# Kernel optimization log

Measured on AMD Instinct MI355X. Metric: run time of the kernel, lower is better.

## Reference

```python
import jax, jax.numpy as jnp
import numpy as np

T, B, IN = 256, 64, 512
HIDDEN = [512, 512, 512]
DILATIONS = [1, 2, 4]


def _lstm_scan(x, W_ih, W_hh, b_ih, b_hh):
    """Run an LSTMCell over leading time axis of x: [Td, N, D] -> [Td, N, H]."""
    H = W_hh.shape[1]
    N = x.shape[1]
    h0 = jnp.zeros((N, H), x.dtype)
    c0 = jnp.zeros((N, H), x.dtype)

    def step(carry, xt):
        h, c = carry
        gates = xt @ W_ih.T + b_ih + h @ W_hh.T + b_hh  # [N, 4H], torch order i,f,g,o
        i, f, g, o = jnp.split(gates, 4, axis=-1)
        c = jax.nn.sigmoid(f) * c + jax.nn.sigmoid(i) * jnp.tanh(g)
        h = jax.nn.sigmoid(o) * jnp.tanh(c)
        return (h, c), h

    _, hs = jax.lax.scan(step, (h0, c0), x)
    return hs


def _drnn_layer(x, rate, W_ih, W_hh, b_ih, b_hh):
    """Dilated RNN layer. x: [T, B, D] with T % rate == 0.
    Torch code concats `rate` consecutive timesteps along batch -> one dilated step;
    reshape [T,B,D] -> [T//rate, rate*B, D] reproduces exactly that layout, and the
    chunk/unroll at the end is the inverse reshape."""
    Tn, Bn, D = x.shape
    Td = Tn // rate
    xd = x.reshape(Td, rate * Bn, D)
    hs = _lstm_scan(xd, W_ih, W_hh, b_ih, b_hh)  # [Td, rate*B, H]
    return hs.reshape(Tn, Bn, W_hh.shape[1])


def setup_inputs() -> dict:
    key = jax.random.key(0)
    ks = jax.random.split(key, 1 + 4 * len(HIDDEN))
    inp = {"x": jax.random.normal(ks[0], (T, B, IN), dtype=jnp.float32)}
    in_dim = IN
    ki = 1
    for li, H in enumerate(HIDDEN):
        bound = 1.0 / np.sqrt(H)
        inp[f"W_ih{li}"] = jax.random.uniform(ks[ki + 0], (4 * H, in_dim), jnp.float32, -bound, bound)
        inp[f"W_hh{li}"] = jax.random.uniform(ks[ki + 1], (4 * H, H), jnp.float32, -bound, bound)
        inp[f"b_ih{li}"] = jax.random.uniform(ks[ki + 2], (4 * H,), jnp.float32, -bound, bound)
        inp[f"b_hh{li}"] = jax.random.uniform(ks[ki + 3], (4 * H,), jnp.float32, -bound, bound)
        ki += 4
        in_dim = H
    return inp


def reference(x,
              W_ih0, W_hh0, b_ih0, b_hh0,
              W_ih1, W_hh1, b_ih1, b_hh1,
              W_ih2, W_hh2, b_ih2, b_hh2):
    params = [(W_ih0, W_hh0, b_ih0, b_hh0),
              (W_ih1, W_hh1, b_ih1, b_hh1),
              (W_ih2, W_hh2, b_ih2, b_hh2)]
    h = x
    for (Wih, Whh, bih, bhh), rate in zip(params, DILATIONS):
        h = _drnn_layer(h, rate, Wih, Whh, bih, bhh)
    return h  # [T, B, HIDDEN[-1]]
```

## Files before the change

### kernel.cpp

```cpp
#include <hip/hip_runtime.h>

typedef __attribute__((ext_vector_type(8))) short bf16x8;
typedef __attribute__((ext_vector_type(4))) float f32x4;

__device__ __forceinline__ unsigned short f2bf(float x) {
    unsigned u = __float_as_uint(x);
    u += 0x7FFFu + ((u >> 16) & 1u);
    return (unsigned short)(u >> 16);
}
__device__ __forceinline__ float sigm(float x) { return 1.0f / (1.0f + __expf(-x)); }
__device__ __forceinline__ float ftanh(float x) {
    float e = __expf(2.f * x);
    return 1.f - 2.f / (e + 1.f);
}

__device__ __forceinline__ void gld16(const unsigned short* g, unsigned short* l) {
    __builtin_amdgcn_global_load_lds((const __attribute__((address_space(1))) void*)g,
                                     (__attribute__((address_space(3))) void*)l, 16, 0, 0);
}

__device__ __forceinline__ void st_plain32(unsigned* p, unsigned v) {
    asm volatile("global_store_dword %0, %1, off" :: "v"(p), "v"(v) : "memory");
}
__device__ __forceinline__ void st_wt32(unsigned* p, unsigned v) {
    asm volatile("global_store_dword %0, %1, off sc0 sc1" :: "v"(p), "v"(v) : "memory");
}
__device__ __forceinline__ void aaddMALL(unsigned* p) {
    unsigned one = 1;
    asm volatile("global_atomic_add %0, %1, off sc1" :: "v"(p), "v"(one) : "memory");
}
__device__ __forceinline__ unsigned ld_mall(const unsigned* p) {
    unsigned v;
    asm volatile("global_load_dword %0, %1, off sc0 sc1\n\ts_waitcnt vmcnt(0)"
                 : "=v"(v) : "v"(p) : "memory");
    return v;
}
__device__ __forceinline__ void st_wt16(unsigned short* p, unsigned v) {
    asm volatile("global_store_short %0, %1, off sc0 sc1" :: "v"(p), "v"(v) : "memory");
}

__device__ __forceinline__ float dppx1(float x) {
    return __int_as_float(__builtin_amdgcn_mov_dpp(__float_as_int(x), 0xB1, 0xF, 0xF, true));
}
__device__ __forceinline__ float dppx2(float x) {
    return __int_as_float(__builtin_amdgcn_mov_dpp(__float_as_int(x), 0x4E, 0xF, 0xF, true));
}

__global__ __launch_bounds__(256) void k_conv_x(const float* __restrict__ x,
                                                unsigned short* __restrict__ Xp) {
    int i = blockIdx.x * 256 + threadIdx.x;
    int rb = i >> 10, kc = (i >> 6) & 15, ln = i & 63;
    int row = (rb << 4) + (ln & 15);
    int k   = (kc << 5) + ((ln >> 4) << 3);
    const float* s = x + (size_t)row * 512 + k;
    float4 v0 = *(const float4*)s, v1 = *(const float4*)(s + 4);
    unsigned short o[8] = {f2bf(v0.x), f2bf(v0.y), f2bf(v0.z), f2bf(v0.w),
                           f2bf(v1.x), f2bf(v1.y), f2bf(v1.z), f2bf(v1.w)};
    *(bf16x8*)(Xp + (size_t)i * 8) = *(bf16x8*)o;
}

__global__ __launch_bounds__(256) void k_conv_w(const float* __restrict__ Wih,
                                                const float* __restrict__ Whh,
                                                unsigned short* __restrict__ Wp) {
    int i = blockIdx.x * 256 + threadIdx.x;
    int wrb = i >> 11, kc = (i >> 6) & 31, ln = i & 63;
    int j = (wrb << 4) + (ln & 15);
    int k = (kc << 5) + ((ln >> 4) << 3);
    int srow = (j & 3) * 512 + (j >> 2);
    const float* s = (k < 512) ? (Wih + (size_t)srow * 512 + k)
                               : (Whh + (size_t)srow * 512 + (k - 512));
    float4 v0 = *(const float4*)s, v1 = *(const float4*)(s + 4);
    unsigned short o[8] = {f2bf(v0.x), f2bf(v0.y), f2bf(v0.z), f2bf(v0.w),
                           f2bf(v1.x), f2bf(v1.y), f2bf(v1.z), f2bf(v1.w)};
    *(bf16x8*)(Wp + (size_t)i * 8) = *(bf16x8*)o;
}

struct DP {
    const unsigned short* Xp;
    unsigned short *Hp0, *Hp1, *Hp2;
    unsigned short *Xq1, *Xq2;
    const unsigned short *Wp0, *Wp1, *Wp2;
    const float *bi0, *bh0, *bi1, *bh1, *bi2, *bh2;
    float* Out;
    unsigned int* flags;
};

__device__ __forceinline__ void quadT(f32x4 a, int sq, float& G0, float& G1, float& G2, float& G3) {
    float a0 = a[0], a1 = a[1], a2 = a[2], a3 = a[3];
    float p1 = (sq & 1) ? a0 : a1; float g1_ = dppx1(p1);
    float p2 = (sq & 1) ? a2 : a3; float g2_ = dppx1(p2);
    float m0 = (sq & 1) ? g1_ : a0, m1 = (sq & 1) ? a1 : g1_;
    float m2 = (sq & 1) ? g2_ : a2, m3 = (sq & 1) ? a3 : g2_;
    float q1 = (sq & 2) ? m0 : m2; float h1_ = dppx2(q1);
    float q2 = (sq & 2) ? m1 : m3; float h2_ = dppx2(q2);
    G0 = (sq & 2) ? h1_ : m0; G1 = (sq & 2) ? h2_ : m1;
    G2 = (sq & 2) ? m2 : h1_; G3 = (sq & 2) ? m3 : h2_;
}

#define PIN8(A,B,C,D,E,F,G,H) \
    asm volatile("" : "+v"(A),"+v"(B),"+v"(C),"+v"(D),"+v"(E),"+v"(F),"+v"(G),"+v"(H))
#define SBAR()  __builtin_amdgcn_sched_barrier(0)
#define MEMBAR() asm volatile("" ::: "memory")
#define RAWBAR() do { MEMBAR(); SBAR(); __builtin_amdgcn_s_barrier(); SBAR(); MEMBAR(); } while (0)

__global__ __launch_bounds__(256, 1) void k_drnn(DP p) {
    const int tid = threadIdx.x, lane = tid & 63, wv = tid >> 6;
    const int l15 = lane & 15, lhi = lane >> 4, sq = l15 & 3;

    const int b = blockIdx.x;
    const int cid = b & 7, w = b >> 3;
    int l, c, T, P, N;
    if (cid < 2)      { l = 0; c = cid;     T = 256; P = 1; N = 64;  }
    else if (cid < 4) { l = 1; c = cid - 2; T = 128; P = 2; N = 128; }
    else              { l = 2; c = cid - 4; T = 64;  P = 2; N = 256; }

    const unsigned short* Xs = (l == 0) ? p.Xp  : (l == 1 ? p.Xq1 : p.Xq2);
    unsigned short*       Hd = (l == 0) ? p.Hp0 : (l == 1 ? p.Hp1 : p.Hp2);
    unsigned short*       Xw = (l == 0) ? p.Xq1 : (l == 1 ? p.Xq2 : nullptr);
    const unsigned short* Ws = (l == 0) ? p.Wp0 : (l == 1 ? p.Wp1 : p.Wp2);
    const float* bi = (l == 0) ? p.bi0 : (l == 1 ? p.bi1 : p.bi2);
    const float* bh = (l == 0) ? p.bh0 : (l == 1 ? p.bh1 : p.bh2);
    const int R0 = c * (P * 32);
    const int alias = (p.Xq1 == p.Hp0);

    __shared__ unsigned short At[65536];
    __shared__ unsigned pollbuf[32];

    const unsigned short* wbase = Ws + ((size_t)(((w << 2) + wv) * 32) << 9) + lane * 8;
#define DECLW(n) bf16x8 w##n = *(const bf16x8*)(wbase + (n << 9));
    DECLW(0) DECLW(1) DECLW(2) DECLW(3) DECLW(4) DECLW(5) DECLW(6) DECLW(7)
    DECLW(8) DECLW(9) DECLW(10) DECLW(11) DECLW(12) DECLW(13) DECLW(14) DECLW(15)
    DECLW(16) DECLW(17) DECLW(18) DECLW(19) DECLW(20) DECLW(21) DECLW(22) DECLW(23)
    DECLW(24) DECLW(25) DECLW(26) DECLW(27) DECLW(28) DECLW(29) DECLW(30) DECLW(31)

    const int hcol = (w << 4) + (wv << 2) + (l15 >> 2);
    const float bs0 = bi[hcol]        + bh[hcol];
    const float bs1 = bi[512 + hcol]  + bh[512 + hcol];
    const float bs2 = bi[1024 + hcol] + bh[1024 + hcol];
    const float bs3 = bi[1536 + hcol] + bh[1536 + hcol];

    const int kch = hcol >> 5;
    const int lane16 = (((hcol & 31) >> 3) << 4) + ((lhi << 2) + sq);
    const int st_lt = lane16 * 8 + (hcol & 7);

    float cst0 = 0.f, cst1 = 0.f, cst2 = 0.f, cst3 = 0.f;
    unsigned int* iflagV = p.flags;
    unsigned int* mflagV = p.flags + 256;
    unsigned int* cflagS = p.flags + 512;
    int fastok = 1;

#define KPX(na, nb, E0, E1, O0, O1, A0, A1) { \
    bf16x8 xa = *(const bf16x8*)((A0) + ((na) << 9)); \
    bf16x8 xb = *(const bf16x8*)((A1) + ((na) << 9)); \
    bf16x8 ya = *(const bf16x8*)((A0) + ((nb) << 9)); \
    bf16x8 yb = *(const bf16x8*)((A1) + ((nb) << 9)); \
    E0 = __builtin_amdgcn_mfma_f32_16x16x32_bf16(xa, w##na, E0, 0, 0, 0); \
    E1 = __builtin_amdgcn_mfma_f32_16x16x32_bf16(xb, w##na, E1, 0, 0, 0); \
    O0 = __builtin_amdgcn_mfma_f32_16x16x32_bf16(ya, w##nb, O0, 0, 0, 0); \
    O1 = __builtin_amdgcn_mfma_f32_16x16x32_bf16(yb, w##nb, O1, 0, 0, 0); }

#define XH(E0, E1, O0, O1, A0, A1) \
    KPX(0,1,E0,E1,O0,O1,A0,A1) KPX(2,3,E0,E1,O0,O1,A0,A1) \
    KPX(4,5,E0,E1,O0,O1,A0,A1) KPX(6,7,E0,E1,O0,O1,A0,A1) \
    KPX(8,9,E0,E1,O0,O1,A0,A1) KPX(10,11,E0,E1,O0,O1,A0,A1) \
    KPX(12,13,E0,E1,O0,O1,A0,A1) KPX(14,15,E0,E1,O0,O1,A0,A1)
#define HH(E0, E1, O0, O1, A0, A1) \
    KPX(16,17,E0,E1,O0,O1,A0,A1) KPX(18,19,E0,E1,O0,O1,A0,A1) \
    KPX(20,21,E0,E1,O0,O1,A0,A1) KPX(22,23,E0,E1,O0,O1,A0,A1) \
    KPX(24,25,E0,E1,O0,O1,A0,A1) KPX(26,27,E0,E1,O0,O1,A0,A1) \
    KPX(28,29,E0,E1,O0,O1,A0,A1) KPX(30,31,E0,E1,O0,O1,A0,A1)

#define PWC(RV, CSTV, HV) { \
    float G0, G1, G2, G3; quadT(RV, sq, G0, G1, G2, G3); \
    float cn = sigm(G1 + bs1) * CSTV + sigm(G0 + bs0) * ftanh(G2 + bs2); \
    HV = sigm(G3 + bs3) * ftanh(cn); CSTV = cn; }

#define STAGE_X(TT) { \
    const int RxN = ((TT) * N + R0) >> 4; \
    for (int i = 0; i < P * 8; ++i) { \
        int q = wv * (P * 8) + i, rb = q >> 4, kc = q & 15; \
        gld16(Xs + ((size_t)((RxN + rb) * 16 + kc) << 9) + lane * 8, \
              &At[(rb * 32 + kc) << 9]); } }
#define STAGE_H(TT) { \
    const int RhN = ((TT) * N + R0) >> 4; \
    for (int i = 0; i < P * 8; ++i) { \
        int q = wv * (P * 8) + i, rb = q >> 4, kc = q & 15; \
        gld16(Hd + ((size_t)((RhN + rb) * 16 + kc) << 9) + lane * 8, \
              &At[(rb * 32 + 16 + kc) << 9]); } }

#define CPOLL(TT) { \
    if (l == 1 && wv == 1 && lane < 2) { \
        const unsigned* cp = cflagS + lane * 32; \
        const unsigned need = 32u * (unsigned)(2 * (TT) + c + 1); \
        int n = 0; \
        while (!__all(ld_mall(cp) >= need)) { if (++n > (1 << 22)) break; } \
    } \
    if (l == 2 && wv == 1 && lane == 0) { \
        const unsigned* cp = cflagS + (2 + (c & 1)) * 32; \
        const unsigned need = 32u * (unsigned)(2 * (TT) + (c >> 1) + 1); \
        int n = 0; \
        while (ld_mall(cp) < need) { if (++n > (1 << 22)) break; } \
    } }

    f32x4 e0 = {0,0,0,0}, e1 = {0,0,0,0}, o0 = {0,0,0,0}, o1 = {0,0,0,0};
    f32x4 e2 = {0,0,0,0}, e3 = {0,0,0,0}, o2 = {0,0,0,0}, o3 = {0,0,0,0};
    const unsigned short* A00 = At + lane * 8;
    const unsigned short* A01 = A00 + (32 << 9);
    const unsigned short* A10 = A00 + (64 << 9);
    const unsigned short* A11 = A00 + (96 << 9);

    if (l > 0) CPOLL(0);
    RAWBAR();
    STAGE_X(0);
    asm volatile("s_waitcnt vmcnt(0)" ::: "memory");
    RAWBAR();
    { XH(e0, e1, o0, o1, A00, A01) }
    if (P == 2) { XH(e2, e3, o2, o3, A10, A11) }

    for (int t = 0; t < T; ++t) {
        PIN8(w0,w1,w2,w3,w4,w5,w6,w7);
        PIN8(w8,w9,w10,w11,w12,w13,w14,w15);
        PIN8(w16,w17,w18,w19,w20,w21,w22,w23);
        PIN8(w24,w25,w26,w27,w28,w29,w30,w31);

        const int RxB = (t * N + R0) >> 4;

        if (t > 0) {
            if (wv == 0) {
                const unsigned need = (unsigned)t;
                const unsigned* mp = mflagV + cid * 32 + (lane & 31);
                if (t == T - 1 || !fastok) {
                    int n = 0;
                    while (!__all(ld_mall(mp) >= need)) { if (++n > (1 << 22)) break; }
                } else {
                    const unsigned short* gip = (const unsigned short*)(iflagV + cid * 32);
                    volatile unsigned* pb = pollbuf;
                    int n = 0;
                    for (;;) {
                        if (lane < 8) gld16(gip + lane * 8, (unsigned short*)pollbuf);
                        asm volatile("s_waitcnt vmcnt(0)" ::: "memory");
                        SBAR();
                        unsigned v = pb[lane & 31];
                        if (__all((v - need) <= 1u)) break;
                        if (++n > 1024) {
                            fastok = 0;
                            int m = 0;
                            while (!__all(ld_mall(mp) >= need)) { if (++m > (1 << 22)) break; }
                            break;
                        }
                    }
                }
            }
            RAWBAR();
            STAGE_H(t - 1);
            asm volatile("s_waitcnt vmcnt(0)" ::: "memory");
            RAWBAR();
            { HH(e0, e1, o0, o1, A00, A01) }
            if (P == 2) { HH(e2, e3, o2, o3, A10, A11) }
        }

        float hv0, hv1, hv2 = 0.f, hv3 = 0.f;
        { f32x4 r0 = e0 + o0, r1 = e1 + o1;
          PWC(r0, cst0, hv0) PWC(r1, cst1, hv1) }
        if (P == 2) {
          f32x4 r2 = e2 + o2, r3 = e3 + o3;
          PWC(r2, cst2, hv2) PWC(r3, cst3, hv3) }

        const unsigned short hb0 = f2bf(hv0), hb1 = f2bf(hv1);
        const unsigned short hb2 = f2bf(hv2), hb3 = f2bf(hv3);
        const size_t i0 = ((size_t)((RxB + 0) * 16 + kch) << 9) + st_lt;
        const size_t i1 = ((size_t)((RxB + 1) * 16 + kch) << 9) + st_lt;
        const size_t i2 = ((size_t)((RxB + 2) * 16 + kch) << 9) + st_lt;
        const size_t i3 = ((size_t)((RxB + 3) * 16 + kch) << 9) + st_lt;
        if (!alias || l == 2) {
            Hd[i0] = hb0; Hd[i1] = hb1;
            if (P == 2) { Hd[i2] = hb2; Hd[i3] = hb3; }
        }
        if (l == 2) {
            p.Out[((size_t)(((RxB + 0) << 4) + (lhi << 2) + sq)) * 512 + hcol] = hv0;
            p.Out[((size_t)(((RxB + 1) << 4) + (lhi << 2) + sq)) * 512 + hcol] = hv1;
            p.Out[((size_t)(((RxB + 2) << 4) + (lhi << 2) + sq)) * 512 + hcol] = hv2;
            p.Out[((size_t)(((RxB + 3) << 4) + (lhi << 2) + sq)) * 512 + hcol] = hv3;
        }
        MEMBAR(); SBAR();
        if (l == 0) { st_wt16(Xw + i0, hb0); st_wt16(Xw + i1, hb1); }
        else if (l == 1) { st_wt16(Xw + i0, hb0); st_wt16(Xw + i1, hb1);
                           st_wt16(Xw + i2, hb2); st_wt16(Xw + i3, hb3); }
        SBAR();
        if (alias && l < 2)  asm volatile("s_waitcnt vmcnt(0)" ::: "memory");
        else if (l == 0)     asm volatile("s_waitcnt vmcnt(2)" ::: "memory");
        else                 asm volatile("s_waitcnt vmcnt(4)" ::: "memory");
        RAWBAR();

        if (t + 1 < T) {
            if (l == 0) {
                STAGE_X(t + 1);
                MEMBAR(); SBAR();
                if (tid == 192) {
                    st_plain32(iflagV + cid * 32 + w, (unsigned)(t + 1));
                    st_wt32(mflagV + cid * 32 + w, (unsigned)(t + 1));
                }
                if (tid == 128 && t > 0) aaddMALL(cflagS + cid * 32);
                SBAR();
                if (wv == 3)                asm volatile("s_waitcnt vmcnt(2)" ::: "memory");
                else if (wv == 2 && t > 0)  asm volatile("s_waitcnt vmcnt(1)" ::: "memory");
                else                        asm volatile("s_waitcnt vmcnt(0)" ::: "memory");
            } else {
                if (tid == 192) {
                    st_plain32(iflagV + cid * 32 + w, (unsigned)(t + 1));
                    st_wt32(mflagV + cid * 32 + w, (unsigned)(t + 1));
                }
                if (tid == 128 && l == 1 && t > 0) aaddMALL(cflagS + cid * 32);
                CPOLL(t + 1);
                RAWBAR();
                STAGE_X(t + 1);
                asm volatile("s_waitcnt vmcnt(0)" ::: "memory");
            }
            RAWBAR();
            e0 = (f32x4){0,0,0,0}; e1 = (f32x4){0,0,0,0};
            o0 = (f32x4){0,0,0,0}; o1 = (f32x4){0,0,0,0};
            { XH(e0, e1, o0, o1, A00, A01) }
            if (P == 2) {
                e2 = (f32x4){0,0,0,0}; e3 = (f32x4){0,0,0,0};
                o2 = (f32x4){0,0,0,0}; o3 = (f32x4){0,0,0,0};
                XH(e2, e3, o2, o3, A10, A11)
            }
        }
    }

    asm volatile("s_waitcnt vmcnt(0)" ::: "memory");
    __builtin_amdgcn_s_barrier();
    if (tid == 192) {
        st_plain32(iflagV + cid * 32 + w, (unsigned)T);
        st_wt32(mflagV + cid * 32 + w, (unsigned)T);
    }
    if (tid == 128 && l < 2) {
        aaddMALL(cflagS + cid * 32);
        aaddMALL(cflagS + cid * 32);
    }
}

extern "C" void kernel_launch(void* const* d_in, const int* in_sizes, int n_in,
                              void* d_out, int out_size, void* d_ws, size_t ws_size,
                              hipStream_t stream)
{
    const float* x = (const float*)d_in[0];
    const float* Wih[3] = {(const float*)d_in[1], (const float*)d_in[5], (const float*)d_in[9]};
    const float* Whh[3] = {(const float*)d_in[2], (const float*)d_in[6], (const float*)d_in[10]};
    const float* bih[3] = {(const float*)d_in[3], (const float*)d_in[7], (const float*)d_in[11]};
    const float* bhh[3] = {(const float*)d_in[4], (const float*)d_in[8], (const float*)d_in[12]};

    char* wp = (char*)d_ws;
    const size_t SZ_A = (size_t)16384 * 512;
    unsigned int* flags = (unsigned int*)wp; wp += 4096;
    unsigned short* Xp  = (unsigned short*)wp; wp += SZ_A * 2;
    unsigned short* Hp0 = (unsigned short*)wp; wp += SZ_A * 2;
    unsigned short* Hp1 = (unsigned short*)wp; wp += SZ_A * 2;
    unsigned short* Hp2 = (unsigned short*)wp; wp += SZ_A * 2;
    unsigned short* Wp[3];
    for (int l = 0; l < 3; ++l) { Wp[l] = (unsigned short*)wp; wp += (size_t)2048 * 1024 * 2; }
    unsigned short* Xq1 = (unsigned short*)wp; wp += SZ_A * 2;
    unsigned short* Xq2 = (unsigned short*)wp; wp += SZ_A * 2;
    const size_t need = (size_t)(wp - (char*)d_ws);
    if (ws_size < need) { Xq1 = Hp0; Xq2 = Hp1; }

    hipMemsetAsync(flags, 0, 4096, stream);
    k_conv_x<<<dim3(4096), dim3(256), 0, stream>>>(x, Xp);
    for (int l = 0; l < 3; ++l)
        k_conv_w<<<dim3(1024), dim3(256), 0, stream>>>(Wih[l], Whh[l], Wp[l]);

    DP dp;
    dp.Xp = Xp; dp.Hp0 = Hp0; dp.Hp1 = Hp1; dp.Hp2 = Hp2;
    dp.Xq1 = Xq1; dp.Xq2 = Xq2;
    dp.Wp0 = Wp[0]; dp.Wp1 = Wp[1]; dp.Wp2 = Wp[2];
    dp.bi0 = bih[0]; dp.bh0 = bhh[0];
    dp.bi1 = bih[1]; dp.bh1 = bhh[1];
    dp.bi2 = bih[2]; dp.bh2 = bhh[2];
    dp.Out = (float*)d_out; dp.flags = flags;

    k_drnn<<<dim3(256), dim3(256), 0, stream>>>(dp);
}
```

Before: 934.2 us.

## Overlap hidden-state handoff stores with next-step X staging and merge barriers

Moves the write-through stores of the new hidden state, which feed the next layer, so they are issued after the next timestep's X staging loads. It also replaces the full drain and barrier after the stores with per-wave partial vmcnt waits and a single barrier. Flag publishing and the cross-layer counter increment are consolidated onto one thread. The goal is to take a barrier and a full memory drain out of the per-step critical path of the serial recurrence, at the cost of fragile hand-counted vmcnt values that must match the exact number of outstanding loads and stores.

Result: faster. 883.0 us (-5.5%).

```diff
diff --git a/kernel.cpp b/kernel.cpp
--- a/kernel.cpp
+++ b/kernel.cpp
@@ -102,6 +102,7 @@
 #define SBAR()  __builtin_amdgcn_sched_barrier(0)
 #define MEMBAR() asm volatile("" ::: "memory")
 #define RAWBAR() do { MEMBAR(); SBAR(); __builtin_amdgcn_s_barrier(); SBAR(); MEMBAR(); } while (0)
+#define VMC(n) asm volatile("s_waitcnt vmcnt(" #n ")" ::: "memory")
 
 __global__ __launch_bounds__(256, 1) void k_drnn(DP p) {
     const int tid = threadIdx.x, lane = tid & 63, wv = tid >> 6;
@@ -212,7 +213,7 @@
     if (l > 0) CPOLL(0);
     RAWBAR();
     STAGE_X(0);
-    asm volatile("s_waitcnt vmcnt(0)" ::: "memory");
+    VMC(0);
     RAWBAR();
     { XH(e0, e1, o0, o1, A00, A01) }
     if (P == 2) { XH(e2, e3, o2, o3, A10, A11) }
@@ -238,7 +239,7 @@
                     int n = 0;
                     for (;;) {
                         if (lane < 8) gld16(gip + lane * 8, (unsigned short*)pollbuf);
-                        asm volatile("s_waitcnt vmcnt(0)" ::: "memory");
+                        VMC(0);
                         SBAR();
                         unsigned v = pb[lane & 31];
                         if (__all((v - need) <= 1u)) break;
@@ -253,7 +254,7 @@
             }
             RAWBAR();
             STAGE_H(t - 1);
-            asm volatile("s_waitcnt vmcnt(0)" ::: "memory");
+            VMC(0);
             RAWBAR();
             { HH(e0, e1, o0, o1, A00, A01) }
             if (P == 2) { HH(e2, e3, o2, o3, A10, A11) }
@@ -272,9 +273,14 @@
         const size_t i1 = ((size_t)((RxB + 1) * 16 + kch) << 9) + st_lt;
         const size_t i2 = ((size_t)((RxB + 2) * 16 + kch) << 9) + st_lt;
         const size_t i3 = ((size_t)((RxB + 3) * 16 + kch) << 9) + st_lt;
+
         if (!alias || l == 2) {
             Hd[i0] = hb0; Hd[i1] = hb1;
             if (P == 2) { Hd[i2] = hb2; Hd[i3] = hb3; }
+        }
+        if (alias && l < 2) {
+            st_wt16(Xw + i0, hb0); st_wt16(Xw + i1, hb1);
+            if (P == 2) { st_wt16(Xw + i2, hb2); st_wt16(Xw + i3, hb3); }
         }
         if (l == 2) {
             p.Out[((size_t)(((RxB + 0) << 4) + (lhi << 2) + sq)) * 512 + hcol] = hv0;
@@ -283,38 +289,49 @@
             p.Out[((size_t)(((RxB + 3) << 4) + (lhi << 2) + sq)) * 512 + hcol] = hv3;
         }
         MEMBAR(); SBAR();
-        if (l == 0) { st_wt16(Xw + i0, hb0); st_wt16(Xw + i1, hb1); }
-        else if (l == 1) { st_wt16(Xw + i0, hb0); st_wt16(Xw + i1, hb1);
-                           st_wt16(Xw + i2, hb2); st_wt16(Xw + i3, hb3); }
-        SBAR();
-        if (alias && l < 2)  asm volatile("s_waitcnt vmcnt(0)" ::: "memory");
-        else if (l == 0)     asm volatile("s_waitcnt vmcnt(2)" ::: "memory");
-        else                 asm volatile("s_waitcnt vmcnt(4)" ::: "memory");
-        RAWBAR();
 
         if (t + 1 < T) {
             if (l == 0) {
+                if (t == 0) RAWBAR();
                 STAGE_X(t + 1);
+                if (!alias) { st_wt16(Xw + i0, hb0); st_wt16(Xw + i1, hb1); }
+                MEMBAR(); SBAR();
+                if (!alias) VMC(10);
+                else        VMC(8);
+                RAWBAR();
+                if (tid == 192) {
+                    st_plain32(iflagV + cid * 32 + w, (unsigned)(t + 1));
+                    st_wt32(mflagV + cid * 32 + w, (unsigned)(t + 1));
+                    if (t > 0) aaddMALL(cflagS + cid * 32);
+                }
+                MEMBAR(); SBAR();
+                if (!alias) {
+                    if (wv == 3) { if (t > 0) VMC(5); else VMC(4); } else VMC(2);
+                } else {
+                    if (wv == 3) { if (t > 0) VMC(3); else VMC(2); } else VMC(0);
+                }
+            } else {
+                CPOLL(t + 1);
+                if (l == 2) VMC(4); else VMC(0);
+                RAWBAR();
+                STAGE_X(t + 1);
+                if (l == 1 && !alias) {
+                    st_wt16(Xw + i0, hb0); st_wt16(Xw + i1, hb1);
+                    st_wt16(Xw + i2, hb2); st_wt16(Xw + i3, hb3);
+                }
                 MEMBAR(); SBAR();
                 if (tid == 192) {
                     st_plain32(iflagV + cid * 32 + w, (unsigned)(t + 1));
                     st_wt32(mflagV + cid * 32 + w, (unsigned)(t + 1));
-                }
-                if (tid == 128 && t > 0) aaddMALL(cflagS + cid * 32);
-                SBAR();
-                if (wv == 3)                asm volatile("s_waitcnt vmcnt(2)" ::: "memory");
-                else if (wv == 2 && t > 0)  asm volatile("s_waitcnt vmcnt(1)" ::: "memory");
-                else                        asm volatile("s_waitcnt vmcnt(0)" ::: "memory");
-            } else {
-                if (tid == 192) {
-                    st_plain32(iflagV + cid * 32 + w, (unsigned)(t + 1));
-                    st_wt32(mflagV + cid * 32 + w, (unsigned)(t + 1));
-                }
-                if (tid == 128 && l == 1 && t > 0) aaddMALL(cflagS + cid * 32);
-                CPOLL(t + 1);
-                RAWBAR();
-                STAGE_X(t + 1);
-                asm volatile("s_waitcnt vmcnt(0)" ::: "memory");
+                    if (l == 1 && t > 0) aaddMALL(cflagS + cid * 32);
+                }
+                MEMBAR(); SBAR();
+                if (l == 1) {
+                    if (!alias) { if (wv == 3) { if (t > 0) VMC(7); else VMC(6); } else VMC(4); }
+                    else        { if (wv == 3) { if (t > 0) VMC(3); else VMC(2); } else VMC(0); }
+                } else {
+                    if (wv == 3) VMC(2); else VMC(0);
+                }
             }
             RAWBAR();
             e0 = (f32x4){0,0,0,0}; e1 = (f32x4){0,0,0,0};
@@ -325,18 +342,22 @@
                 o2 = (f32x4){0,0,0,0}; o3 = (f32x4){0,0,0,0};
                 XH(e2, e3, o2, o3, A10, A11)
             }
+        } else {
+            if (!alias && l == 0) { st_wt16(Xw + i0, hb0); st_wt16(Xw + i1, hb1); }
+            if (!alias && l == 1) { st_wt16(Xw + i0, hb0); st_wt16(Xw + i1, hb1);
+                                    st_wt16(Xw + i2, hb2); st_wt16(Xw + i3, hb3); }
+            MEMBAR(); SBAR();
+            VMC(0);
+            RAWBAR();
         }
     }
 
-    asm volatile("s_waitcnt vmcnt(0)" ::: "memory");
+    VMC(0);
     __builtin_amdgcn_s_barrier();
     if (tid == 192) {
         st_plain32(iflagV + cid * 32 + w, (unsigned)T);
         st_wt32(mflagV + cid * 32 + w, (unsigned)T);
-    }
-    if (tid == 128 && l < 2) {
-        aaddMALL(cflagS + cid * 32);
-        aaddMALL(cflagS + cid * 32);
+        if (l < 2) { aaddMALL(cflagS + cid * 32); aaddMALL(cflagS + cid * 32); }
     }
 }
 
```
